# Optimization experiments

Measured on AMD Instinct MI355X. Metric: run time of the kernel, lower is better.

## Reference

```python
import jax, jax.numpy as jnp
import numpy as np

# Dims: batch=2, seqlen=L=384, d_inner=d=384, d_state=s=384, dt_rank=r=384, d_conv=4.
# NOTE: the original torch module only runs when L == d_inner == d_state == dt_rank
# (see its broadcasting in SelectiveScan and the Linear layer plumbing); we reproduce
# that exact (quirky) broadcast faithfully.
B_, L_, D_, S_, R_, K_ = 2, 384, 384, 384, 384, 4


def setup_inputs() -> dict:
    key = jax.random.key(0)
    ks = jax.random.split(key, 9)
    f32 = jnp.float32
    return {
        "x": jax.random.normal(ks[0], (B_, L_, D_), f32),
        "A_log": jax.random.normal(ks[1], (D_, S_), f32) * 0.02,
        "D": jax.random.normal(ks[2], (D_,), f32) * 0.02,
        "dt_w": jax.random.normal(ks[3], (D_, R_), f32) * 0.02,
        "dt_b": jax.random.normal(ks[4], (D_,), f32) * 0.02,
        "B_w": jax.random.normal(ks[5], (S_, D_), f32) * (1.0 / np.sqrt(D_)),
        "C_w": jax.random.normal(ks[6], (S_, D_), f32) * (1.0 / np.sqrt(D_)),
        "conv_w": jax.random.normal(ks[7], (D_, 1, K_), f32) * (1.0 / np.sqrt(K_)),
        "conv_b": jnp.zeros((D_,), f32),
    }


def _forward(x, A_log, D, dt_w, dt_b, B_w, C_w, conv_w, conv_b):
    b, L, d = x.shape
    A = -jnp.exp(A_log)                       # (d, s)
    dt = jax.nn.softplus(x @ dt_w.T + dt_b)   # (b, L, d)
    x_dbl = x @ B_w.T                         # (b, L, s)
    Bm = x_dbl @ B_w.T                        # (b, L, s)  (module applies B_proj twice)
    Cm = x_dbl @ C_w.T                        # (b, L, s)
    # causal depthwise conv1d: pad (k-1) on the left == torch pad k-1 then [:, :, :L]
    xc = jax.lax.conv_general_dilated(
        x.transpose(0, 2, 1), conv_w, (1,), [(conv_w.shape[-1] - 1, 0)],
        feature_group_count=d, dimension_numbers=("NCH", "OIH", "NCH"))
    xc = xc + conv_b[None, :, None]
    u = jax.nn.silu(xc.transpose(0, 2, 1))    # (b, L, d)
    # selective scan (faithful to the torch SelectiveScan broadcasting)
    deltaA = jnp.exp(dt[..., None] * A[None, None])          # (b, L, d, s)
    deltaB_u = dt[..., None] * Bm[:, None, :, :] * u[..., None]  # (b, L, d, s), needs L==d

    def step(h, inp):
        dA_i, dBu_i, C_i, u_i = inp
        h = dA_i * h + dBu_i                  # (b, d, s)
        y = jnp.sum(h * C_i[:, None, :], -1) + u_i * D  # (b, d)
        return h, y

    h0 = jnp.zeros((b, d, deltaA.shape[-1]), x.dtype)
    xs = (deltaA.transpose(1, 0, 2, 3), deltaB_u.transpose(1, 0, 2, 3),
          Cm.transpose(1, 0, 2), u.transpose(1, 0, 2))
    _, ys = jax.lax.scan(step, h0, xs)        # ys: (L, b, d)
    return ys.transpose(1, 0, 2)


def reference(x, A_log, D, dt_w, dt_b, B_w, C_w, conv_w, conv_b):
    return _forward(x, A_log, D, dt_w, dt_b, B_w, C_w, conv_w, conv_b)
```

## Files before the change

kernel.cpp:

```cpp
#include <hip/hip_runtime.h>
#include <math.h>

#define B_SZ 2
#define L_SZ 384
#define D_SZ 384
#define S_SZ 384
#define BLK_ELEMS (L_SZ * D_SZ)
#define TOT_ELEMS (B_SZ * L_SZ * D_SZ)
#define LOG2E 1.4426950408889634f

typedef __attribute__((ext_vector_type(8))) short bf16x8;
typedef __attribute__((ext_vector_type(4))) float f32x4;

__device__ __forceinline__ float fexp2(float x) {
  return __builtin_amdgcn_exp2f(x);
}
__device__ __forceinline__ float softplus_f(float z) {
  return (z > 20.f) ? z : log1pf(__expf(z));
}
__device__ __forceinline__ unsigned short f2bf(float f) {
  unsigned int u = __float_as_uint(f);
  return (unsigned short)((u + 0x7FFFu + ((u >> 16) & 1u)) >> 16);
}
#define PIPELINE_FENCE() asm volatile("" ::: "memory")

template <int CTRL>
__device__ __forceinline__ float dpp_mov(float v) {
  return __int_as_float(
      __builtin_amdgcn_update_dpp(0, __float_as_int(v), CTRL, 0xF, 0xF, true));
}

__global__ __launch_bounds__(256) void cvt_bf16_kernel(
    const float* __restrict__ x, const float* __restrict__ dt_w,
    const float* __restrict__ B_w, const float* __restrict__ C_w,
    unsigned short* __restrict__ xbf, unsigned short* __restrict__ dtwbf,
    unsigned short* __restrict__ Bwbf, unsigned short* __restrict__ Cwbf) {
  const int blk = blockIdx.x;
  const float* src;
  unsigned short* dst;
  int base;
  if (blk < 288) { src = x; dst = xbf; base = blk; }
  else if (blk < 432) { src = dt_w; dst = dtwbf; base = blk - 288; }
  else if (blk < 576) { src = B_w; dst = Bwbf; base = blk - 432; }
  else { src = C_w; dst = Cwbf; base = blk - 576; }
  const int idx = base * 1024 + threadIdx.x * 4;
  const float4 v = *(const float4*)(src + idx);
  ushort4 o;
  o.x = f2bf(v.x); o.y = f2bf(v.y); o.z = f2bf(v.z); o.w = f2bf(v.w);
  *(ushort4*)(dst + idx) = o;
}

template <int MODE>
__global__ __launch_bounds__(128, 2) void mfma_dual_gemm(
    const unsigned short* __restrict__ Abf,
    const unsigned short* __restrict__ W1bf,
    const unsigned short* __restrict__ W2bf,
    const float* __restrict__ bias,
    float* __restrict__ O1, void* __restrict__ O2v) {
  __shared__ unsigned short sA[32 * 392];
  __shared__ unsigned short sW1[16 * 392];
  __shared__ unsigned short sW2[16 * 392];

  const int t = threadIdx.x;
  const int wv = t >> 6;
  const int lane = t & 63;
  const int nt = blockIdx.x;
  const int mrow = blockIdx.y;

  const unsigned short* Ab = Abf + mrow * 32 * 384;
  const unsigned short* W1b = W1bf + nt * 16 * 384;
  const unsigned short* W2b = W2bf + nt * 16 * 384;

#pragma unroll
  for (int it = 0; it < 12; ++it) {
    const int id = t + it * 128;
    const int row = id / 48, col = id - row * 48;
    *(bf16x8*)&sA[row * 392 + col * 8] = *(const bf16x8*)(Ab + id * 8);
  }
#pragma unroll
  for (int it = 0; it < 6; ++it) {
    const int id = t + it * 128;
    const int row = id / 48, col = id - row * 48;
    *(bf16x8*)&sW1[row * 392 + col * 8] = *(const bf16x8*)(W1b + id * 8);
    *(bf16x8*)&sW2[row * 392 + col * 8] = *(const bf16x8*)(W2b + id * 8);
  }
  __syncthreads();

  const int rc = lane & 15;
  const int quad = lane >> 4;
  bf16x8 af[12], w1f[12], w2f[12];
#pragma unroll
  for (int kt = 0; kt < 12; ++kt) {
    af[kt] = *(const bf16x8*)&sA[(wv * 16 + rc) * 392 + quad * 8 + kt * 32];
    w1f[kt] = *(const bf16x8*)&sW1[rc * 392 + quad * 8 + kt * 32];
    w2f[kt] = *(const bf16x8*)&sW2[rc * 392 + quad * 8 + kt * 32];
  }
  PIPELINE_FENCE();
  f32x4 acc1 = {0.f, 0.f, 0.f, 0.f};
  f32x4 acc2 = {0.f, 0.f, 0.f, 0.f};
#pragma unroll
  for (int kt = 0; kt < 12; ++kt) {
    acc1 = __builtin_amdgcn_mfma_f32_16x16x32_bf16(af[kt], w1f[kt], acc1, 0, 0, 0);
    acc2 = __builtin_amdgcn_mfma_f32_16x16x32_bf16(af[kt], w2f[kt], acc2, 0, 0, 0);
  }
  const int col = nt * 16 + rc;
  const int row0 = mrow * 32 + wv * 16 + quad * 4;
  if constexpr (MODE == 1) {
    unsigned short* O2 = (unsigned short*)O2v;
    const float bb = bias[col];
#pragma unroll
    for (int r = 0; r < 4; ++r) {
      O1[(row0 + r) * 384 + col] = softplus_f(acc1[r] + bb);
      O2[(row0 + r) * 384 + col] = f2bf(acc2[r]);
    }
  } else {
    float* O2 = (float*)O2v;
#pragma unroll
    for (int r = 0; r < 4; ++r) {
      O1[(row0 + r) * 384 + col] = acc1[r];
      O2[(row0 + r) * 384 + col] = acc2[r];
    }
  }
}

__global__ __launch_bounds__(256) void conv_tr_kernel(
    const float* __restrict__ x, const float* __restrict__ cw,
    const float* __restrict__ cb, const float* __restrict__ dt,
    float* __restrict__ u, float* __restrict__ dt_t,
    float* __restrict__ dtu_t) {
  __shared__ float Tdt[32][33];
  __shared__ float Tdu[32][33];
  const int tx = threadIdx.x;
  const int ty = threadIdx.y;
  const int b = blockIdx.z;
  const int i0 = blockIdx.y * 32;
  const int l0 = blockIdx.x * 32;
  const int gi = i0 + tx;
  const float cbv = cb[gi];
  const float cw0 = cw[gi * 4 + 0], cw1 = cw[gi * 4 + 1];
  const float cw2 = cw[gi * 4 + 2], cw3 = cw[gi * 4 + 3];
#pragma unroll
  for (int r = 0; r < 4; ++r) {
    const int l = l0 + ty + 8 * r;
    float acc = cbv;
    const float x3 = x[(b * L_SZ + l) * D_SZ + gi];
    const float x2 = (l >= 1) ? x[(b * L_SZ + l - 1) * D_SZ + gi] : 0.f;
    const float x1 = (l >= 2) ? x[(b * L_SZ + l - 2) * D_SZ + gi] : 0.f;
    const float x0 = (l >= 3) ? x[(b * L_SZ + l - 3) * D_SZ + gi] : 0.f;
    acc = fmaf(x0, cw0, acc);
    acc = fmaf(x1, cw1, acc);
    acc = fmaf(x2, cw2, acc);
    acc = fmaf(x3, cw3, acc);
    const float uv = acc / (1.f + __expf(-acc));
    const int off = (b * L_SZ + l) * D_SZ + gi;
    u[off] = uv;
    const float dtv = dt[off];
    Tdt[ty + 8 * r][tx] = dtv;
    Tdu[ty + 8 * r][tx] = dtv * uv;
  }
  __syncthreads();
#pragma unroll
  for (int r = 0; r < 4; ++r) {
    const int il = ty + 8 * r;
    const int off = (b * D_SZ + i0 + il) * L_SZ + l0 + tx;
    dt_t[off] = Tdt[tx][il];
    dtu_t[off] = Tdu[tx][il];
  }
}

struct ChunkS {
  f32x4 d0, d1, u0, u1;
  float c[8];
};

#define LOAD_CHUNK(K, B0, B1, B2, DTB, DUB)                                    \
  {                                                                            \
    asm volatile("global_load_dwordx4 %0, %1, off" : "=v"(K.d0) : "v"(DTB));   \
    asm volatile("global_load_dwordx4 %0, %1, off offset:16"                   \
                 : "=v"(K.d1) : "v"(DTB));                                     \
    asm volatile("global_load_dwordx4 %0, %1, off" : "=v"(K.u0) : "v"(DUB));   \
    asm volatile("global_load_dwordx4 %0, %1, off offset:16"                   \
                 : "=v"(K.u1) : "v"(DUB));                                     \
    asm volatile("global_load_dword %0, %1, off" : "=v"(K.c[0]) : "v"(B0));    \
    asm volatile("global_load_dword %0, %1, off offset:1536"                   \
                 : "=v"(K.c[1]) : "v"(B0));                                    \
    asm volatile("global_load_dword %0, %1, off offset:3072"                   \
                 : "=v"(K.c[2]) : "v"(B0));                                    \
    asm volatile("global_load_dword %0, %1, off" : "=v"(K.c[3]) : "v"(B1));    \
    asm volatile("global_load_dword %0, %1, off offset:1536"                   \
                 : "=v"(K.c[4]) : "v"(B1));                                    \
    asm volatile("global_load_dword %0, %1, off offset:3072"                   \
                 : "=v"(K.c[5]) : "v"(B1));                                    \
    asm volatile("global_load_dword %0, %1, off" : "=v"(K.c[6]) : "v"(B2));    \
    asm volatile("global_load_dword %0, %1, off offset:1536"                   \
                 : "=v"(K.c[7]) : "v"(B2));                                    \
  }

#define WAIT_CHUNK(K)                                                          \
  asm volatile("s_waitcnt vmcnt(24)"                                           \
               : "+v"(K.d0), "+v"(K.d1), "+v"(K.u0), "+v"(K.u1),               \
                 "+v"(K.c[0]), "+v"(K.c[1]), "+v"(K.c[2]), "+v"(K.c[3]),       \
                 "+v"(K.c[4]), "+v"(K.c[5]), "+v"(K.c[6]), "+v"(K.c[7]))

#define ADV_BASES()                                                            \
  { cb0 += 3072; cb1 += 3072; cb2 += 3072; dtB += 8; duB += 8; }

__global__ __launch_bounds__(64, 4) void scan_kernel(
    const float* __restrict__ A_log, const float* __restrict__ dt_t,
    const float* __restrict__ dtu_t, const float* __restrict__ Bm,
    const float* __restrict__ Cm, float* __restrict__ part) {
  const int wave = blockIdx.x;
  const int lane = threadIdx.x;
  const int w = wave % 6;
  const int sid = wave / 6;
  const int b = sid / D_SZ;
  const int i = sid % D_SZ;
  const int j = w * 64 + lane;

  const float a2 = -__expf(A_log[i * S_SZ + j]) * LOG2E;
  const float bw = Bm[(b * D_SZ + i) * S_SZ + j];
  float h = 0.f;

  const float* dtB = dt_t + (b * D_SZ + i) * L_SZ;
  const float* duB = dtu_t + (b * D_SZ + i) * L_SZ;
  const float* cmrow = Cm + b * BLK_ELEMS + j;
  const float* cb0 = cmrow;
  const float* cb1 = cmrow + 3 * D_SZ;
  const float* cb2 = cmrow + 6 * D_SZ;

  const int sq = (((lane >> 3) & 1) << 2) | (((lane >> 2) & 1) << 1) | (lane & 1);
  const bool storer = (lane & 0x32) == 0;
  float* pstore = part + ((w * B_SZ + b) * D_SZ + i) * L_SZ + sq;

  asm volatile("" :: "v"(a2), "v"(bw));
  asm volatile("s_waitcnt vmcnt(0)");

  auto compute_chunk = [&](ChunkS& K) {
    float acc[8];
    const float dts[8] = {K.d0[0], K.d0[1], K.d0[2], K.d0[3],
                          K.d1[0], K.d1[1], K.d1[2], K.d1[3]};
    const float dus[8] = {K.u0[0], K.u0[1], K.u0[2], K.u0[3],
                          K.u1[0], K.u1[1], K.u1[2], K.u1[3]};
#pragma unroll
    for (int s = 0; s < 8; ++s) {
      const float e = fexp2(dts[s] * a2);
      h = fmaf(e, h, bw * dus[s]);
      acc[s] = h * K.c[s];
    }
    {
      const bool hi = (lane & 8) != 0;
#pragma unroll
      for (int q = 0; q < 4; ++q) {
        const float keep = hi ? acc[q + 4] : acc[q];
        const float send = hi ? acc[q] : acc[q + 4];
        acc[q] = keep + dpp_mov<0x140>(send);
      }
    }
    {
      const bool hi = (lane & 4) != 0;
#pragma unroll
      for (int q = 0; q < 2; ++q) {
        const float keep = hi ? acc[q + 2] : acc[q];
        const float send = hi ? acc[q] : acc[q + 2];
        acc[q] = keep + dpp_mov<0x141>(send);
      }
    }
    {
      const bool hi = (lane & 1) != 0;
      const float keep = hi ? acc[1] : acc[0];
      const float send = hi ? acc[0] : acc[1];
      acc[0] = keep + dpp_mov<0xB1>(send);
    }
    float r = acc[0];
    r += __shfl_xor(r, 2, 64);
    r += __shfl_xor(r, 16, 64);
    r += __shfl_xor(r, 32, 64);
    if (storer) *pstore = r;
    pstore += 8;
  };

  ChunkS K0, K1, K2;
  LOAD_CHUNK(K0, cb0, cb1, cb2, dtB, duB);
  ADV_BASES();
  LOAD_CHUNK(K1, cb0, cb1, cb2, dtB, duB);
  ADV_BASES();
#pragma unroll 1
  for (int it = 0; it < 16; ++it) {
    LOAD_CHUNK(K2, cb0, cb1, cb2, dtB, duB);
    ADV_BASES();
    WAIT_CHUNK(K0);
    compute_chunk(K0);
    LOAD_CHUNK(K0, cb0, cb1, cb2, dtB, duB);
    ADV_BASES();
    WAIT_CHUNK(K1);
    compute_chunk(K1);
    LOAD_CHUNK(K1, cb0, cb1, cb2, dtB, duB);
    ADV_BASES();
    WAIT_CHUNK(K2);
    compute_chunk(K2);
  }
}

__global__ __launch_bounds__(256) void combine_kernel(
    const float* __restrict__ part, const float* __restrict__ u,
    const float* __restrict__ Dv, float* __restrict__ y) {
  __shared__ float T[32][33];
  const int tx = threadIdx.x;
  const int ty0 = threadIdx.y;
  const int b = blockIdx.z;
  const int i0 = blockIdx.y * 32;
  const int l0 = blockIdx.x * 32;
#pragma unroll
  for (int r = 0; r < 4; ++r) {
    const int il = ty0 + 8 * r;
    float s = 0.f;
#pragma unroll
    for (int w = 0; w < 6; ++w)
      s += part[((w * B_SZ + b) * D_SZ + i0 + il) * L_SZ + l0 + tx];
    T[il][tx] = s;
  }
  __syncthreads();
#pragma unroll
  for (int r = 0; r < 4; ++r) {
    const int ll = ty0 + 8 * r;
    const int gi = i0 + tx;
    const int off = (b * L_SZ + l0 + ll) * D_SZ + gi;
    y[off] = fmaf(u[off], Dv[gi], T[tx][ll]);
  }
}

extern "C" void kernel_launch(void* const* d_in, const int* in_sizes, int n_in,
                              void* d_out, int out_size, void* d_ws,
                              size_t ws_size, hipStream_t stream) {
  const float* x = (const float*)d_in[0];
  const float* A_log = (const float*)d_in[1];
  const float* D = (const float*)d_in[2];
  const float* dt_w = (const float*)d_in[3];
  const float* dt_b = (const float*)d_in[4];
  const float* B_w = (const float*)d_in[5];
  const float* C_w = (const float*)d_in[6];
  const float* conv_w = (const float*)d_in[7];
  const float* conv_b = (const float*)d_in[8];
  float* y = (float*)d_out;

  float* ws = (float*)d_ws;
  float* dt = ws;
  float* u = ws + TOT_ELEMS;
  float* Bm = ws + 2 * TOT_ELEMS;
  float* Cm = ws + 3 * TOT_ELEMS;
  float* dt_t = ws + 4 * TOT_ELEMS;
  float* dtu_t = ws + 5 * TOT_ELEMS;
  float* part = ws + 6 * TOT_ELEMS;
  unsigned short* bfarea = (unsigned short*)(ws + 12 * TOT_ELEMS);
  unsigned short* xbf = bfarea;
  unsigned short* dtwbf = bfarea + 294912;
  unsigned short* Bwbf = bfarea + 442368;
  unsigned short* Cwbf = bfarea + 589824;
  unsigned short* xdblbf = bfarea + 737280;

  cvt_bf16_kernel<<<720, 256, 0, stream>>>(x, dt_w, B_w, C_w, xbf, dtwbf, Bwbf, Cwbf);
  mfma_dual_gemm<1><<<dim3(24, 24), 128, 0, stream>>>(xbf, dtwbf, Bwbf, dt_b, dt, xdblbf);
  mfma_dual_gemm<2><<<dim3(24, 24), 128, 0, stream>>>(xdblbf, Bwbf, Cwbf, nullptr, Bm, Cm);
  conv_tr_kernel<<<dim3(L_SZ / 32, D_SZ / 32, B_SZ), dim3(32, 8), 0, stream>>>(
      x, conv_w, conv_b, dt, u, dt_t, dtu_t);
  scan_kernel<<<6 * B_SZ * D_SZ, 64, 0, stream>>>(A_log, dt_t, dtu_t, Bm, Cm, part);
  combine_kernel<<<dim3(L_SZ / 32, D_SZ / 32, B_SZ), dim3(32, 8), 0, stream>>>(
      part, u, D, y);
}
```

Before: 138.9 us.

## Fuse conv into prep kernel, write dt transposed from GEMM, compute dt*u in scan

The depthwise conv and SiLU, along with the u transpose, move into the bf16 conversion kernel, which removes one launch. The first GEMM now writes softplus(dt) straight into the transposed layout the scan needs, so the separate dt transpose and the dt*u buffer are gone. The scan forms dt*u inline. The GEMM also stages tiles with direct global-to-LDS loads and no padding, which may bring LDS bank conflicts and uncoalesced transposed stores from the GEMM epilogue.

```diff
diff --git a/kernel.cpp b/kernel.cpp
--- a/kernel.cpp
+++ b/kernel.cpp
@@ -24,117 +24,49 @@
 }
 #define PIPELINE_FENCE() asm volatile("" ::: "memory")
 
+__device__ __forceinline__ void g2l16(const void* g, void* l) {
+  __builtin_amdgcn_global_load_lds(
+      (const __attribute__((address_space(1))) unsigned int*)g,
+      (__attribute__((address_space(3))) unsigned int*)l, 16, 0, 0);
+}
+
 template <int CTRL>
 __device__ __forceinline__ float dpp_mov(float v) {
   return __int_as_float(
       __builtin_amdgcn_update_dpp(0, __float_as_int(v), CTRL, 0xF, 0xF, true));
 }
 
-__global__ __launch_bounds__(256) void cvt_bf16_kernel(
+__global__ __launch_bounds__(256) void prep_kernel(
     const float* __restrict__ x, const float* __restrict__ dt_w,
     const float* __restrict__ B_w, const float* __restrict__ C_w,
+    const float* __restrict__ cw, const float* __restrict__ cb,
     unsigned short* __restrict__ xbf, unsigned short* __restrict__ dtwbf,
-    unsigned short* __restrict__ Bwbf, unsigned short* __restrict__ Cwbf) {
+    unsigned short* __restrict__ Bwbf, unsigned short* __restrict__ Cwbf,
+    float* __restrict__ u, float* __restrict__ u_t) {
+  __shared__ float Tu[32][33];
   const int blk = blockIdx.x;
-  const float* src;
-  unsigned short* dst;
-  int base;
-  if (blk < 288) { src = x; dst = xbf; base = blk; }
-  else if (blk < 432) { src = dt_w; dst = dtwbf; base = blk - 288; }
-  else if (blk < 576) { src = B_w; dst = Bwbf; base = blk - 432; }
-  else { src = C_w; dst = Cwbf; base = blk - 576; }
-  const int idx = base * 1024 + threadIdx.x * 4;
-  const float4 v = *(const float4*)(src + idx);
-  ushort4 o;
-  o.x = f2bf(v.x); o.y = f2bf(v.y); o.z = f2bf(v.z); o.w = f2bf(v.w);
-  *(ushort4*)(dst + idx) = o;
-}
-
-template <int MODE>
-__global__ __launch_bounds__(128, 2) void mfma_dual_gemm(
-    const unsigned short* __restrict__ Abf,
-    const unsigned short* __restrict__ W1bf,
-    const unsigned short* __restrict__ W2bf,
-    const float* __restrict__ bias,
-    float* __restrict__ O1, void* __restrict__ O2v) {
-  __shared__ unsigned short sA[32 * 392];
-  __shared__ unsigned short sW1[16 * 392];
-  __shared__ unsigned short sW2[16 * 392];
-
-  const int t = threadIdx.x;
-  const int wv = t >> 6;
-  const int lane = t & 63;
-  const int nt = blockIdx.x;
-  const int mrow = blockIdx.y;
-
-  const unsigned short* Ab = Abf + mrow * 32 * 384;
-  const unsigned short* W1b = W1bf + nt * 16 * 384;
-  const unsigned short* W2b = W2bf + nt * 16 * 384;
-
-#pragma unroll
-  for (int it = 0; it < 12; ++it) {
-    const int id = t + it * 128;
-    const int row = id / 48, col = id - row * 48;
-    *(bf16x8*)&sA[row * 392 + col * 8] = *(const bf16x8*)(Ab + id * 8);
-  }
-#pragma unroll
-  for (int it = 0; it < 6; ++it) {
-    const int id = t + it * 128;
-    const int row = id / 48, col = id - row * 48;
-    *(bf16x8*)&sW1[row * 392 + col * 8] = *(const bf16x8*)(W1b + id * 8);
-    *(bf16x8*)&sW2[row * 392 + col * 8] = *(const bf16x8*)(W2b + id * 8);
-  }
-  __syncthreads();
-
-  const int rc = lane & 15;
-  const int quad = lane >> 4;
-  bf16x8 af[12], w1f[12], w2f[12];
-#pragma unroll
-  for (int kt = 0; kt < 12; ++kt) {
-    af[kt] = *(const bf16x8*)&sA[(wv * 16 + rc) * 392 + quad * 8 + kt * 32];
-    w1f[kt] = *(const bf16x8*)&sW1[rc * 392 + quad * 8 + kt * 32];
-    w2f[kt] = *(const bf16x8*)&sW2[rc * 392 + quad * 8 + kt * 32];
-  }
-  PIPELINE_FENCE();
-  f32x4 acc1 = {0.f, 0.f, 0.f, 0.f};
-  f32x4 acc2 = {0.f, 0.f, 0.f, 0.f};
-#pragma unroll
-  for (int kt = 0; kt < 12; ++kt) {
-    acc1 = __builtin_amdgcn_mfma_f32_16x16x32_bf16(af[kt], w1f[kt], acc1, 0, 0, 0);
-    acc2 = __builtin_amdgcn_mfma_f32_16x16x32_bf16(af[kt], w2f[kt], acc2, 0, 0, 0);
-  }
-  const int col = nt * 16 + rc;
-  const int row0 = mrow * 32 + wv * 16 + quad * 4;
-  if constexpr (MODE == 1) {
-    unsigned short* O2 = (unsigned short*)O2v;
-    const float bb = bias[col];
-#pragma unroll
-    for (int r = 0; r < 4; ++r) {
-      O1[(row0 + r) * 384 + col] = softplus_f(acc1[r] + bb);
-      O2[(row0 + r) * 384 + col] = f2bf(acc2[r]);
-    }
-  } else {
-    float* O2 = (float*)O2v;
-#pragma unroll
-    for (int r = 0; r < 4; ++r) {
-      O1[(row0 + r) * 384 + col] = acc1[r];
-      O2[(row0 + r) * 384 + col] = acc2[r];
-    }
-  }
-}
-
-__global__ __launch_bounds__(256) void conv_tr_kernel(
-    const float* __restrict__ x, const float* __restrict__ cw,
-    const float* __restrict__ cb, const float* __restrict__ dt,
-    float* __restrict__ u, float* __restrict__ dt_t,
-    float* __restrict__ dtu_t) {
-  __shared__ float Tdt[32][33];
-  __shared__ float Tdu[32][33];
-  const int tx = threadIdx.x;
-  const int ty = threadIdx.y;
-  const int b = blockIdx.z;
-  const int i0 = blockIdx.y * 32;
-  const int l0 = blockIdx.x * 32;
+  if (blk < 720) {
+    const float* src;
+    unsigned short* dst;
+    int base;
+    if (blk < 288) { src = x; dst = xbf; base = blk; }
+    else if (blk < 432) { src = dt_w; dst = dtwbf; base = blk - 288; }
+    else if (blk < 576) { src = B_w; dst = Bwbf; base = blk - 432; }
+    else { src = C_w; dst = Cwbf; base = blk - 576; }
+    const int idx = base * 1024 + threadIdx.x * 4;
+    const float4 v = *(const float4*)(src + idx);
+    ushort4 o;
+    o.x = f2bf(v.x); o.y = f2bf(v.y); o.z = f2bf(v.z); o.w = f2bf(v.w);
+    *(ushort4*)(dst + idx) = o;
+    return;
+  }
+  const int cblk = blk - 720;
+  const int b = cblk / 144;
+  const int rem = cblk % 144;
+  const int iy = rem / 12, lx = rem % 12;
+  const int tx = threadIdx.x & 31;
+  const int ty = threadIdx.x >> 5;
+  const int i0 = iy * 32, l0 = lx * 32;
   const int gi = i0 + tx;
   const float cbv = cb[gi];
   const float cw0 = cw[gi * 4 + 0], cw1 = cw[gi * 4 + 1];
@@ -152,19 +84,87 @@
     acc = fmaf(x2, cw2, acc);
     acc = fmaf(x3, cw3, acc);
     const float uv = acc / (1.f + __expf(-acc));
-    const int off = (b * L_SZ + l) * D_SZ + gi;
-    u[off] = uv;
-    const float dtv = dt[off];
-    Tdt[ty + 8 * r][tx] = dtv;
-    Tdu[ty + 8 * r][tx] = dtv * uv;
+    u[(b * L_SZ + l) * D_SZ + gi] = uv;
+    Tu[ty + 8 * r][tx] = uv;
   }
   __syncthreads();
 #pragma unroll
   for (int r = 0; r < 4; ++r) {
     const int il = ty + 8 * r;
-    const int off = (b * D_SZ + i0 + il) * L_SZ + l0 + tx;
-    dt_t[off] = Tdt[tx][il];
-    dtu_t[off] = Tdu[tx][il];
+    u_t[(b * D_SZ + i0 + il) * L_SZ + l0 + tx] = Tu[tx][il];
+  }
+}
+
+template <int MODE>
+__global__ __launch_bounds__(128, 2) void mfma_dual_gemm(
+    const unsigned short* __restrict__ Abf,
+    const unsigned short* __restrict__ W1bf,
+    const unsigned short* __restrict__ W2bf,
+    const float* __restrict__ bias,
+    float* __restrict__ O1, void* __restrict__ O2v) {
+  __shared__ unsigned short sA[32 * 384];
+  __shared__ unsigned short sW1[16 * 384];
+  __shared__ unsigned short sW2[16 * 384];
+
+  const int t = threadIdx.x;
+  const int wv = t >> 6;
+  const int lane = t & 63;
+  const int nt = blockIdx.x;
+  const int mrow = blockIdx.y;
+
+  const unsigned short* Ab = Abf + mrow * 32 * 384;
+  const unsigned short* W1b = W1bf + nt * 16 * 384;
+  const unsigned short* W2b = W2bf + nt * 16 * 384;
+
+#pragma unroll
+  for (int it = 0; it < 12; ++it) {
+    const int id = t + it * 128;
+    g2l16(Ab + id * 8, (char*)sA + id * 16);
+  }
+#pragma unroll
+  for (int it = 0; it < 6; ++it) {
+    const int id = t + it * 128;
+    g2l16(W1b + id * 8, (char*)sW1 + id * 16);
+    g2l16(W2b + id * 8, (char*)sW2 + id * 16);
+  }
+  __syncthreads();
+
+  const int rc = lane & 15;
+  const int quad = lane >> 4;
+  bf16x8 af[12], w1f[12], w2f[12];
+#pragma unroll
+  for (int kt = 0; kt < 12; ++kt) {
+    af[kt] = *(const bf16x8*)&sA[(wv * 16 + rc) * 384 + kt * 32 + quad * 8];
+    w1f[kt] = *(const bf16x8*)&sW1[rc * 384 + kt * 32 + quad * 8];
+    w2f[kt] = *(const bf16x8*)&sW2[rc * 384 + kt * 32 + quad * 8];
+  }
+  PIPELINE_FENCE();
+  f32x4 acc1 = {0.f, 0.f, 0.f, 0.f};
+  f32x4 acc2 = {0.f, 0.f, 0.f, 0.f};
+#pragma unroll
+  for (int kt = 0; kt < 12; ++kt) {
+    acc1 = __builtin_amdgcn_mfma_f32_16x16x32_bf16(af[kt], w1f[kt], acc1, 0, 0, 0);
+    acc2 = __builtin_amdgcn_mfma_f32_16x16x32_bf16(af[kt], w2f[kt], acc2, 0, 0, 0);
+  }
+  const int col = nt * 16 + rc;
+  const int row0 = mrow * 32 + wv * 16 + quad * 4;
+  if constexpr (MODE == 1) {
+    unsigned short* O2 = (unsigned short*)O2v;
+    const float bb = bias[col];
+    const int b = row0 / L_SZ;
+    const int lb = row0 - b * L_SZ;
+#pragma unroll
+    for (int r = 0; r < 4; ++r) {
+      O1[(b * D_SZ + col) * L_SZ + lb + r] = softplus_f(acc1[r] + bb);
+      O2[(row0 + r) * 384 + col] = f2bf(acc2[r]);
+    }
+  } else {
+    float* O2 = (float*)O2v;
+#pragma unroll
+    for (int r = 0; r < 4; ++r) {
+      O1[(row0 + r) * 384 + col] = acc1[r];
+      O2[(row0 + r) * 384 + col] = acc2[r];
+    }
   }
 }
 
@@ -207,7 +207,7 @@
 
 __global__ __launch_bounds__(64, 4) void scan_kernel(
     const float* __restrict__ A_log, const float* __restrict__ dt_t,
-    const float* __restrict__ dtu_t, const float* __restrict__ Bm,
+    const float* __restrict__ u_t, const float* __restrict__ Bm,
     const float* __restrict__ Cm, float* __restrict__ part) {
   const int wave = blockIdx.x;
   const int lane = threadIdx.x;
@@ -222,7 +222,7 @@
   float h = 0.f;
 
   const float* dtB = dt_t + (b * D_SZ + i) * L_SZ;
-  const float* duB = dtu_t + (b * D_SZ + i) * L_SZ;
+  const float* duB = u_t + (b * D_SZ + i) * L_SZ;
   const float* cmrow = Cm + b * BLK_ELEMS + j;
   const float* cb0 = cmrow;
   const float* cb1 = cmrow + 3 * D_SZ;
@@ -239,12 +239,12 @@
     float acc[8];
     const float dts[8] = {K.d0[0], K.d0[1], K.d0[2], K.d0[3],
                           K.d1[0], K.d1[1], K.d1[2], K.d1[3]};
-    const float dus[8] = {K.u0[0], K.u0[1], K.u0[2], K.u0[3],
-                          K.u1[0], K.u1[1], K.u1[2], K.u1[3]};
+    const float us[8] = {K.u0[0], K.u0[1], K.u0[2], K.u0[3],
+                         K.u1[0], K.u1[1], K.u1[2], K.u1[3]};
 #pragma unroll
     for (int s = 0; s < 8; ++s) {
       const float e = fexp2(dts[s] * a2);
-      h = fmaf(e, h, bw * dus[s]);
+      h = fmaf(e, h, bw * (dts[s] * us[s]));
       acc[s] = h * K.c[s];
     }
     {
@@ -344,26 +344,26 @@
   float* y = (float*)d_out;
 
   float* ws = (float*)d_ws;
-  float* dt = ws;
-  float* u = ws + TOT_ELEMS;
-  float* Bm = ws + 2 * TOT_ELEMS;
-  float* Cm = ws + 3 * TOT_ELEMS;
-  float* dt_t = ws + 4 * TOT_ELEMS;
-  float* dtu_t = ws + 5 * TOT_ELEMS;
-  float* part = ws + 6 * TOT_ELEMS;
-  unsigned short* bfarea = (unsigned short*)(ws + 12 * TOT_ELEMS);
+  float* u = ws;
+  float* Bm = ws + TOT_ELEMS;
+  float* Cm = ws + 2 * TOT_ELEMS;
+  float* dt_t = ws + 3 * TOT_ELEMS;
+  float* u_t = ws + 4 * TOT_ELEMS;
+  float* part = ws + 5 * TOT_ELEMS;
+  unsigned short* bfarea = (unsigned short*)(ws + 11 * TOT_ELEMS);
   unsigned short* xbf = bfarea;
   unsigned short* dtwbf = bfarea + 294912;
   unsigned short* Bwbf = bfarea + 442368;
   unsigned short* Cwbf = bfarea + 589824;
   unsigned short* xdblbf = bfarea + 737280;
 
-  cvt_bf16_kernel<<<720, 256, 0, stream>>>(x, dt_w, B_w, C_w, xbf, dtwbf, Bwbf, Cwbf);
-  mfma_dual_gemm<1><<<dim3(24, 24), 128, 0, stream>>>(xbf, dtwbf, Bwbf, dt_b, dt, xdblbf);
-  mfma_dual_gemm<2><<<dim3(24, 24), 128, 0, stream>>>(xdblbf, Bwbf, Cwbf, nullptr, Bm, Cm);
-  conv_tr_kernel<<<dim3(L_SZ / 32, D_SZ / 32, B_SZ), dim3(32, 8), 0, stream>>>(
-      x, conv_w, conv_b, dt, u, dt_t, dtu_t);
-  scan_kernel<<<6 * B_SZ * D_SZ, 64, 0, stream>>>(A_log, dt_t, dtu_t, Bm, Cm, part);
+  prep_kernel<<<1008, 256, 0, stream>>>(x, dt_w, B_w, C_w, conv_w, conv_b,
+                                        xbf, dtwbf, Bwbf, Cwbf, u, u_t);
+  mfma_dual_gemm<1><<<dim3(24, 24), 128, 0, stream>>>(xbf, dtwbf, Bwbf, dt_b,
+                                                      dt_t, xdblbf);
+  mfma_dual_gemm<2><<<dim3(24, 24), 128, 0, stream>>>(xdblbf, Bwbf, Cwbf,
+                                                      nullptr, Bm, Cm);
+  scan_kernel<<<6 * B_SZ * D_SZ, 64, 0, stream>>>(A_log, dt_t, u_t, Bm, Cm, part);
   combine_kernel<<<dim3(L_SZ / 32, D_SZ / 32, B_SZ), dim3(32, 8), 0, stream>>>(
       part, u, D, y);
 }
```

New measurement: 139.7 us. About the same (+0.5%).
